# Performance work log

Measured on AMD Instinct MI355X. Metric: run time of the kernel, lower is better.

The kernel has to match this reference:

```python
import jax, jax.numpy as jnp
import numpy as np

N_TOTAL = 2_000_000   # total particles across all events
N_EVENTS = 20_000     # number of events (segments)
H = 64                # phi/rho hidden width
OUT = 10              # output classes


def _lin(x, W, b):
    # torch nn.Linear: y = x @ W.T + b
    return x @ W.T + b


def setup_inputs() -> dict:
    key = jax.random.key(0)
    ks = jax.random.split(key, 24)
    s = 0.1  # small init scale
    inp = {
        "values": jax.random.normal(ks[0], (N_TOTAL,), dtype=jnp.float32),
        "seg_ids": jnp.sort(jax.random.randint(ks[1], (N_TOTAL,), 0, N_EVENTS)),
        "p1w0": jax.random.normal(ks[2], (H, 1), dtype=jnp.float32) * s,
        "p1b0": jax.random.normal(ks[3], (H,), dtype=jnp.float32) * s,
        "p1w1": jax.random.normal(ks[4], (H, H), dtype=jnp.float32) * s,
        "p1b1": jax.random.normal(ks[5], (H,), dtype=jnp.float32) * s,
        "r1w0": jax.random.normal(ks[6], (H, H), dtype=jnp.float32) * s,
        "r1b0": jax.random.normal(ks[7], (H,), dtype=jnp.float32) * s,
        "r1w1": jax.random.normal(ks[8], (H, H), dtype=jnp.float32) * s,
        "r1b1": jax.random.normal(ks[9], (H,), dtype=jnp.float32) * s,
        "o1w": jax.random.normal(ks[10], (H, H), dtype=jnp.float32) * s,
        "o1b": jax.random.normal(ks[11], (H,), dtype=jnp.float32) * s,
        "p2w0": jax.random.normal(ks[12], (H, H), dtype=jnp.float32) * s,
        "p2b0": jax.random.normal(ks[13], (H,), dtype=jnp.float32) * s,
        "p2w1": jax.random.normal(ks[14], (H, H), dtype=jnp.float32) * s,
        "p2b1": jax.random.normal(ks[15], (H,), dtype=jnp.float32) * s,
        "r2w0": jax.random.normal(ks[16], (H, H), dtype=jnp.float32) * s,
        "r2b0": jax.random.normal(ks[17], (H,), dtype=jnp.float32) * s,
        "r2w1": jax.random.normal(ks[18], (H, H), dtype=jnp.float32) * s,
        "r2b1": jax.random.normal(ks[19], (H,), dtype=jnp.float32) * s,
        "o2w": jax.random.normal(ks[20], (OUT, H), dtype=jnp.float32) * s,
        "o2b": jax.random.normal(ks[21], (OUT,), dtype=jnp.float32) * s,
    }
    return inp


def reference(values, seg_ids, p1w0, p1b0, p1w1, p1b1, r1w0, r1b0, r1w1, r1b1,
              o1w, o1b, p2w0, p2b0, p2w1, p2b1, r2w0, r2b0, r2w1, r2b1, o2w, o2b):
    relu = jax.nn.relu
    # stage 1: phi1 on each scalar particle value -> [N, H]
    h = relu(_lin(values[:, None], p1w0, p1b0))
    h = relu(_lin(h, p1w1, p1b1))
    # jagged sum over particles within each event (the inner deepset sum)
    ev = jax.ops.segment_sum(h, seg_ids, num_segments=N_EVENTS)  # [E, H]
    # rho1 + output linear + activation per event
    ev = relu(_lin(ev, r1w0, r1b0))
    ev = relu(_lin(ev, r1w1, r1b1))
    ev = relu(_lin(ev, o1w, o1b))  # [E, H] (output_size of deepset1 = rho_sizes[-1])
    # stage 2: phi2 per event, sum over all events
    h2 = relu(_lin(ev, p2w0, p2b0))
    h2 = relu(_lin(h2, p2w1, p2b1))
    s2 = jnp.sum(h2, axis=0, keepdims=True)  # [1, H]
    r2 = relu(_lin(s2, r2w0, r2b0))
    r2 = relu(_lin(r2, r2w1, r2b1))
    out = _lin(r2, o2w, o2b)  # [1, OUT]
    return jax.nn.log_softmax(out, axis=1)
```

## Files before the change

### kernel.cpp

```cpp
#include <hip/hip_runtime.h>

#define NT 2000000
#define NE 20000
#define NT4 (NT / 4)
#define K1_BLOCKS 2048
#define K1_WAVES (K1_BLOCKS * 4)
#define K2_BLOCKS ((NE + 63) / 64)
#define NSEG 65
#define K0_BLOCKS ((NT4 + 255) / 256)

using half8  = __attribute__((ext_vector_type(8))) _Float16;
using half2v = __attribute__((ext_vector_type(2))) _Float16;
using f32x4  = __attribute__((ext_vector_type(4))) float;
using fvec4  = __attribute__((ext_vector_type(4))) float;

__device__ __forceinline__ half8 load_h8(const float* __restrict__ p) {
    fvec4 a = *(const fvec4*)p;
    fvec4 b = *(const fvec4*)(p + 4);
    half8 r;
#pragma unroll
    for (int e = 0; e < 4; e++) {
        r[e]     = (_Float16)a[e];
        r[e + 4] = (_Float16)b[e];
    }
    return r;
}

__global__ __launch_bounds__(256) void k0_fused(
    const int* __restrict__ seg, int* __restrict__ off, float* __restrict__ s2,
    int* __restrict__ counter,
    const float* __restrict__ w0, const float* __restrict__ b0,
    const float* __restrict__ w1, const float* __restrict__ b1,
    float* __restrict__ sorted_t, half2v* __restrict__ tabg) {
    if (blockIdx.x < NSEG) {
        __shared__ float tS[64], w0S[64], b0S[64];
        __shared__ int rankS_unused[1];
        __shared__ int styleS[64];
        const int k = threadIdx.x;
        float t = 0.f; int rank = 0;
        if (k < 64) {
            const float w = w0[k], b = b0[k];
            int style;
            if (w != 0.f) { t = -b / w; style = (w > 0.f) ? 1 : 0; }
            else          { t = (b > 0.f) ? -INFINITY : INFINITY; style = 1; }
            tS[k] = t; w0S[k] = w; b0S[k] = b; styleS[k] = style;
        }
        __syncthreads();
        if (k < 64) {
            for (int i = 0; i < 64; i++) {
                const float ti = tS[i];
                rank += (ti < t || (ti == t && i < k)) ? 1 : 0;
            }
        }
        __syncthreads();
        __shared__ int rankS[64];
        if (k < 64) rankS[k] = rank;
        __syncthreads();
        if (k < 64) {
            if (blockIdx.x == 0) sorted_t[rank] = t;
            const int s = blockIdx.x;
            float a = 0.f, c = b1[k];
            for (int kk = 0; kk < 64; kk++) {
                const bool act = styleS[kk] ? (s > rankS[kk]) : (s <= rankS[kk]);
                if (act) {
                    const float wjk = w1[k * 64 + kk];
                    a = fmaf(wjk, w0S[kk], a);
                    c = fmaf(wjk, b0S[kk], c);
                }
            }
            tabg[s * 64 + k] = half2v{(_Float16)a, (_Float16)c};
        }
    }

    if (blockIdx.x == 0) {
        if (threadIdx.x < 64) s2[threadIdx.x] = 0.f;
        if (threadIdx.x == 64) *counter = 0;
    }
    const int g = blockIdx.x * 256 + threadIdx.x;
    if (g >= NT4) return;
    const int idx4 = g * 4;
    const int4 s = *(const int4*)(seg + idx4);
    int prev = (g == 0) ? -1 : seg[idx4 - 1];
    int vals[4] = {s.x, s.y, s.z, s.w};
#pragma unroll
    for (int k = 0; k < 4; k++) {
        const int cur = vals[k];
        if (cur != prev) {
            for (int e = prev + 1; e <= cur; ++e) off[e] = idx4 + k;
        }
        prev = cur;
    }
    if (idx4 + 3 == NT - 1) {
        for (int e = prev + 1; e <= NE; ++e) off[e] = NT;
    }
}

__global__ __launch_bounds__(256) void k1_phi1(
    const float* __restrict__ values, const int* __restrict__ off,
    const float* __restrict__ sorted_t, const half2v* __restrict__ gtab,
    float* __restrict__ ev) {
    __shared__ __align__(16) half2v tab[NSEG * 64];
    const int tid = threadIdx.x;
    const int w = tid >> 6, l = tid & 63;

    for (int idx = tid; idx < NSEG * 64; idx += 256) tab[idx] = gtab[idx];
    const float t_l = sorted_t[l];
    __syncthreads();

    const int wid = blockIdx.x * 4 + w;
    for (int e = wid; e < NE; e += K1_WAVES) {
        const int ps = off[e], pe = off[e + 1];
        float a0 = 0.f, a1 = 0.f, a2 = 0.f, a3 = 0.f;

        for (int base = ps; base < pe; base += 64) {
            const int cnt = min(pe - base, 64);
            const float v_l = (base + l < pe) ? values[base + l] : 0.f;
            const int v_li = __float_as_int(v_l);

            auto PROC = [&](int i, float& acc) {
                const float vs =
                    __int_as_float(__builtin_amdgcn_readlane(v_li, i));
                const int sg = (int)__popcll(__ballot(vs > t_l));
                const half2v ac = tab[sg * 64 + l];
                acc += fmaxf(fmaf((float)ac[0], vs, (float)ac[1]), 0.f);
            };

            const int full = cnt >> 2;
#pragma unroll
            for (int g = 0; g < 16; ++g) {
                if (g >= full) break;
                PROC(4 * g,     a0);
                PROC(4 * g + 1, a1);
                PROC(4 * g + 2, a2);
                PROC(4 * g + 3, a3);
            }
            const int tb = full * 4;
            if (tb     < cnt) PROC(tb,     a0);
            if (tb + 1 < cnt) PROC(tb + 1, a1);
            if (tb + 2 < cnt) PROC(tb + 2, a2);
        }
        ev[(size_t)e * 64 + l] = (a0 + a1) + (a2 + a3);
    }
}

__global__ __launch_bounds__(64) void k2_events(
    const float* __restrict__ ev,
    const float* __restrict__ W0, const float* __restrict__ B0,
    const float* __restrict__ W1, const float* __restrict__ B1,
    const float* __restrict__ W2, const float* __restrict__ B2,
    const float* __restrict__ W3, const float* __restrict__ B3,
    const float* __restrict__ W4, const float* __restrict__ B4,
    float* __restrict__ s2, int* __restrict__ counter,
    const float* __restrict__ R0, const float* __restrict__ Rb0,
    const float* __restrict__ R1, const float* __restrict__ Rb1,
    const float* __restrict__ OW, const float* __restrict__ OB,
    float* __restrict__ out) {
    __shared__ __align__(16) _Float16 xt[64 * 72];
    const int l   = threadIdx.x;
    const int l15 = l & 15;
    const int l4  = l >> 4;
    const int ebase = blockIdx.x * 64;

    const float* Ws[5] = {W0, W1, W2, W3, W4};
    const float* Bs[5] = {B0, B1, B2, B3, B4};

    half8 A[4][2];
#pragma unroll
    for (int pf = 0; pf < 4; pf++) {
        const int e = ebase + pf * 16 + l15;
#pragma unroll
        for (int kf = 0; kf < 2; kf++) {
            half8 a;
            if (e < NE) {
                a = load_h8(ev + (size_t)e * 64 + kf * 32 + l4 * 8);
            } else {
#pragma unroll
                for (int e2 = 0; e2 < 8; e2++) a[e2] = (_Float16)0.f;
            }
            A[pf][kf] = a;
        }
    }

#pragma unroll
    for (int L = 0; L < 5; L++) {
        half8 Bh[2][4];
#pragma unroll
        for (int kf = 0; kf < 2; kf++)
#pragma unroll
            for (int jf = 0; jf < 4; jf++)
                Bh[kf][jf] = load_h8(Ws[L] + (jf * 16 + l15) * 64 +
                                     kf * 32 + l4 * 8);

        f32x4 acc[4][4];
#pragma unroll
        for (int jf = 0; jf < 4; jf++) {
            const float bj = Bs[L][jf * 16 + l15];
#pragma unroll
            for (int pf = 0; pf < 4; pf++)
#pragma unroll
                for (int r = 0; r < 4; r++) acc[pf][jf][r] = bj;
        }
#pragma unroll
        for (int kf = 0; kf < 2; kf++)
#pragma unroll
            for (int pf = 0; pf < 4; pf++)
#pragma unroll
                for (int jf = 0; jf < 4; jf++)
                    acc[pf][jf] = __builtin_amdgcn_mfma_f32_16x16x32_f16(
                        A[pf][kf], Bh[kf][jf], acc[pf][jf], 0, 0, 0);

        if (L < 4) {
#pragma unroll
            for (int pf = 0; pf < 4; pf++)
#pragma unroll
                for (int jf = 0; jf < 4; jf++) {
                    const int j = jf * 16 + l15;
#pragma unroll
                    for (int r = 0; r < 4; r++)
                        xt[(pf * 16 + l4 * 4 + r) * 72 + j] =
                            (_Float16)fmaxf(acc[pf][jf][r], 0.f);
                }
#pragma unroll
            for (int pf = 0; pf < 4; pf++)
#pragma unroll
                for (int kf = 0; kf < 2; kf++)
                    A[pf][kf] = *(const half8*)(xt + (pf * 16 + l15) * 72 +
                                                kf * 32 + l4 * 8);
        } else {
            float sj[4];
#pragma unroll
            for (int jf = 0; jf < 4; jf++) {
                float s = 0.f;
#pragma unroll
                for (int pf = 0; pf < 4; pf++)
#pragma unroll
                    for (int r = 0; r < 4; r++) {
                        const int e = ebase + pf * 16 + l4 * 4 + r;
                        float v = fmaxf(acc[pf][jf][r], 0.f);
                        s += (e < NE) ? v : 0.f;
                    }
                s += __shfl_xor(s, 16);
                s += __shfl_xor(s, 32);
                sj[jf] = s;
            }
            float v = (l4 == 0) ? sj[0] : (l4 == 1) ? sj[1]
                    : (l4 == 2) ? sj[2] : sj[3];
            atomicAdd(s2 + l, v);
        }
    }

    __shared__ int is_last;
    __threadfence();
    if (l == 0) {
        const int c = atomicAdd(counter, 1);
        is_last = (c == (int)gridDim.x - 1);
    }
    __syncthreads();
    if (!is_last) return;

    __shared__ __align__(16) float xb[64];
    __shared__ __align__(16) float yb[64];
    __shared__ float ob[10];

    xb[l] = atomicAdd(s2 + l, 0.f);
    __syncthreads();

    float a0 = Rb0[l];
#pragma unroll
    for (int k = 0; k < 16; k++) {
        fvec4 wv = *(const fvec4*)(R0 + l * 64 + k * 4);
        fvec4 xv = *(const fvec4*)(xb + k * 4);
        a0 += wv[0] * xv[0] + wv[1] * xv[1] + wv[2] * xv[2] + wv[3] * xv[3];
    }
    yb[l] = fmaxf(a0, 0.f);
    __syncthreads();

    float b_ = Rb1[l];
#pragma unroll
    for (int k = 0; k < 16; k++) {
        fvec4 wv = *(const fvec4*)(R1 + l * 64 + k * 4);
        fvec4 xv = *(const fvec4*)(yb + k * 4);
        b_ += wv[0] * xv[0] + wv[1] * xv[1] + wv[2] * xv[2] + wv[3] * xv[3];
    }
    __syncthreads();
    xb[l] = fmaxf(b_, 0.f);
    __syncthreads();

    if (l < 10) {
        float o = OB[l];
#pragma unroll
        for (int k = 0; k < 16; k++) {
            fvec4 wv = *(const fvec4*)(OW + l * 64 + k * 4);
            fvec4 xv = *(const fvec4*)(xb + k * 4);
            o += wv[0] * xv[0] + wv[1] * xv[1] + wv[2] * xv[2] + wv[3] * xv[3];
        }
        ob[l] = o;
    }
    __syncthreads();
    if (l == 0) {
        float m = ob[0];
#pragma unroll
        for (int i = 1; i < 10; i++) m = fmaxf(m, ob[i]);
        float sum = 0.f;
#pragma unroll
        for (int i = 0; i < 10; i++) sum = sum + expf(ob[i] - m);
        float ls = logf(sum);
#pragma unroll
        for (int i = 0; i < 10; i++) out[i] = ob[i] - m - ls;
    }
}

extern "C" void kernel_launch(void* const* d_in, const int* in_sizes, int n_in,
                              void* d_out, int out_size, void* d_ws, size_t ws_size,
                              hipStream_t stream) {
    const float* values = (const float*)d_in[0];
    const int*   seg    = (const int*)d_in[1];
    const float* p1w0 = (const float*)d_in[2],  *p1b0 = (const float*)d_in[3];
    const float* p1w1 = (const float*)d_in[4],  *p1b1 = (const float*)d_in[5];
    const float* r1w0 = (const float*)d_in[6],  *r1b0 = (const float*)d_in[7];
    const float* r1w1 = (const float*)d_in[8],  *r1b1 = (const float*)d_in[9];
    const float* o1w  = (const float*)d_in[10], *o1b  = (const float*)d_in[11];
    const float* p2w0 = (const float*)d_in[12], *p2b0 = (const float*)d_in[13];
    const float* p2w1 = (const float*)d_in[14], *p2b1 = (const float*)d_in[15];
    const float* r2w0 = (const float*)d_in[16], *r2b0 = (const float*)d_in[17];
    const float* r2w1 = (const float*)d_in[18], *r2b1 = (const float*)d_in[19];
    const float* o2w  = (const float*)d_in[20], *o2b  = (const float*)d_in[21];

    float*  ev       = (float*)d_ws;
    float*  s2       = ev + (size_t)NE * 64;
    int*    off      = (int*)(s2 + 64);
    int*    counter  = off + (NE + 1);
    float*  sorted_t = (float*)(counter + 1);
    half2v* tabg     = (half2v*)(sorted_t + 64);

    hipLaunchKernelGGL(k0_fused, dim3(K0_BLOCKS), dim3(256), 0, stream,
                       seg, off, s2, counter,
                       p1w0, p1b0, p1w1, p1b1, sorted_t, tabg);
    hipLaunchKernelGGL(k1_phi1, dim3(K1_BLOCKS), dim3(256), 0, stream,
                       values, off, sorted_t, tabg, ev);
    hipLaunchKernelGGL(k2_events, dim3(K2_BLOCKS), dim3(64), 0, stream,
                       ev, r1w0, r1b0, r1w1, r1b1, o1w, o1b,
                       p2w0, p2b0, p2w1, p2b1, s2, counter,
                       r2w0, r2b0, r2w1, r2b1, o2w, o2b, (float*)d_out);
}
```

Before: 74.52 us.

## Process two particles per wave step with half-wave hidden-unit split

```diff
diff --git a/kernel.cpp b/kernel.cpp
--- a/kernel.cpp
+++ b/kernel.cpp
@@ -10,7 +10,7 @@
 #define K0_BLOCKS ((NT4 + 255) / 256)
 
 using half8  = __attribute__((ext_vector_type(8))) _Float16;
-using half2v = __attribute__((ext_vector_type(2))) _Float16;
+using half4v = __attribute__((ext_vector_type(4))) _Float16;
 using f32x4  = __attribute__((ext_vector_type(4))) float;
 using fvec4  = __attribute__((ext_vector_type(4))) float;
 
@@ -31,11 +31,10 @@
     int* __restrict__ counter,
     const float* __restrict__ w0, const float* __restrict__ b0,
     const float* __restrict__ w1, const float* __restrict__ b1,
-    float* __restrict__ sorted_t, half2v* __restrict__ tabg) {
+    float* __restrict__ sorted_t, half4v* __restrict__ tabg) {
     if (blockIdx.x < NSEG) {
-        __shared__ float tS[64], w0S[64], b0S[64];
-        __shared__ int rankS_unused[1];
-        __shared__ int styleS[64];
+        __shared__ float tS[64], w0S[64], b0S[64], aS[64], cS[64];
+        __shared__ int styleS[64], rankS[64];
         const int k = threadIdx.x;
         float t = 0.f; int rank = 0;
         if (k < 64) {
@@ -51,10 +50,8 @@
                 const float ti = tS[i];
                 rank += (ti < t || (ti == t && i < k)) ? 1 : 0;
             }
-        }
-        __syncthreads();
-        __shared__ int rankS[64];
-        if (k < 64) rankS[k] = rank;
+            rankS[k] = rank;
+        }
         __syncthreads();
         if (k < 64) {
             if (blockIdx.x == 0) sorted_t[rank] = t;
@@ -68,7 +65,14 @@
                     c = fmaf(wjk, b0S[kk], c);
                 }
             }
-            tabg[s * 64 + k] = half2v{(_Float16)a, (_Float16)c};
+            aS[k] = a; cS[k] = c;
+        }
+        __syncthreads();
+        if (k < 32) {
+            const int s = blockIdx.x;
+            tabg[s * 32 + k] = half4v{
+                (_Float16)aS[2 * k],     (_Float16)cS[2 * k],
+                (_Float16)aS[2 * k + 1], (_Float16)cS[2 * k + 1]};
         }
     }
 
@@ -97,49 +101,75 @@
 
 __global__ __launch_bounds__(256) void k1_phi1(
     const float* __restrict__ values, const int* __restrict__ off,
-    const float* __restrict__ sorted_t, const half2v* __restrict__ gtab,
+    const float* __restrict__ sorted_t, const half4v* __restrict__ gtab,
     float* __restrict__ ev) {
-    __shared__ __align__(16) half2v tab[NSEG * 64];
+    __shared__ __align__(16) half4v tab[NSEG * 32];
     const int tid = threadIdx.x;
     const int w = tid >> 6, l = tid & 63;
-
-    for (int idx = tid; idx < NSEG * 64; idx += 256) tab[idx] = gtab[idx];
+    const int l31 = l & 31;
+    const bool lo32 = (l < 32);
+
+    for (int idx = tid; idx < NSEG * 32; idx += 256) tab[idx] = gtab[idx];
     const float t_l = sorted_t[l];
     __syncthreads();
 
     const int wid = blockIdx.x * 4 + w;
     for (int e = wid; e < NE; e += K1_WAVES) {
         const int ps = off[e], pe = off[e + 1];
-        float a0 = 0.f, a1 = 0.f, a2 = 0.f, a3 = 0.f;
+        float2 p0 = {0.f, 0.f}, p1 = {0.f, 0.f};
+        float2 p2 = {0.f, 0.f}, p3 = {0.f, 0.f};
 
         for (int base = ps; base < pe; base += 64) {
             const int cnt = min(pe - base, 64);
             const float v_l = (base + l < pe) ? values[base + l] : 0.f;
             const int v_li = __float_as_int(v_l);
 
-            auto PROC = [&](int i, float& acc) {
-                const float vs =
+            auto PROC2 = [&](int i, int j, float2& acc) {
+                const float vsA =
                     __int_as_float(__builtin_amdgcn_readlane(v_li, i));
-                const int sg = (int)__popcll(__ballot(vs > t_l));
-                const half2v ac = tab[sg * 64 + l];
-                acc += fmaxf(fmaf((float)ac[0], vs, (float)ac[1]), 0.f);
+                const float vsB =
+                    __int_as_float(__builtin_amdgcn_readlane(v_li, j));
+                const int sgA = (int)__popcll(__ballot(vsA > t_l));
+                const int sgB = (int)__popcll(__ballot(vsB > t_l));
+                const int sg  = lo32 ? sgA : sgB;
+                const float vs = lo32 ? vsA : vsB;
+                const half4v ac = tab[sg * 32 + l31];
+                acc.x += fmaxf(fmaf((float)ac[0], vs, (float)ac[1]), 0.f);
+                acc.y += fmaxf(fmaf((float)ac[2], vs, (float)ac[3]), 0.f);
             };
-
-            const int full = cnt >> 2;
-#pragma unroll
-            for (int g = 0; g < 16; ++g) {
-                if (g >= full) break;
-                PROC(4 * g,     a0);
-                PROC(4 * g + 1, a1);
-                PROC(4 * g + 2, a2);
-                PROC(4 * g + 3, a3);
-            }
-            const int tb = full * 4;
-            if (tb     < cnt) PROC(tb,     a0);
-            if (tb + 1 < cnt) PROC(tb + 1, a1);
-            if (tb + 2 < cnt) PROC(tb + 2, a2);
-        }
-        ev[(size_t)e * 64 + l] = (a0 + a1) + (a2 + a3);
+            auto PROC1 = [&](int i, float2& acc) {
+                const float vsA =
+                    __int_as_float(__builtin_amdgcn_readlane(v_li, i));
+                const int sgA = (int)__popcll(__ballot(vsA > t_l));
+                const half4v ac = tab[sgA * 32 + l31];
+                const float x = fmaxf(fmaf((float)ac[0], vsA, (float)ac[1]), 0.f);
+                const float y = fmaxf(fmaf((float)ac[2], vsA, (float)ac[3]), 0.f);
+                acc.x += lo32 ? x : 0.f;
+                acc.y += lo32 ? y : 0.f;
+            };
+
+            const int fullg = cnt >> 3;
+#pragma unroll
+            for (int g = 0; g < 8; ++g) {
+                if (g >= fullg) break;
+                PROC2(8 * g,     8 * g + 1, p0);
+                PROC2(8 * g + 2, 8 * g + 3, p1);
+                PROC2(8 * g + 4, 8 * g + 5, p2);
+                PROC2(8 * g + 6, 8 * g + 7, p3);
+            }
+            int tb = fullg * 8;
+            if (tb + 1 < cnt) { PROC2(tb, tb + 1, p0); tb += 2; }
+            if (tb + 1 < cnt) { PROC2(tb, tb + 1, p1); tb += 2; }
+            if (tb + 1 < cnt) { PROC2(tb, tb + 1, p2); tb += 2; }
+            if (tb < cnt)     { PROC1(tb, p3); }
+        }
+
+        float s0 = (p0.x + p1.x) + (p2.x + p3.x);
+        float s1 = (p0.y + p1.y) + (p2.y + p3.y);
+        s0 += __shfl_xor(s0, 32);
+        s1 += __shfl_xor(s1, 32);
+        if (lo32)
+            *(float2*)(ev + (size_t)e * 64 + 2 * l31) = make_float2(s0, s1);
     }
 }
 
@@ -331,7 +361,7 @@
     int*    off      = (int*)(s2 + 64);
     int*    counter  = off + (NE + 1);
     float*  sorted_t = (float*)(counter + 1);
-    half2v* tabg     = (half2v*)(sorted_t + 64);
+    half4v* tabg     = (half4v*)(sorted_t + 64);
 
     hipLaunchKernelGGL(k0_fused, dim3(K0_BLOCKS), dim3(256), 0, stream,
                        seg, off, s2, counter,
```

New measurement: 74.49 us. Within noise of the previous version (-0.0%).
